# Optimization experiments

Hardware: AMD Instinct MI355X
Metric: run time of the kernel (lower is better)

The kernel has to match this reference:

```python
import jax, jax.numpy as jnp
import numpy as np
import math

LN_EPS = 1e-5

def _ln(x, g, b):
    m = jnp.mean(x, -1, keepdims=True)
    v = jnp.mean((x - m) ** 2, -1, keepdims=True)
    return (x - m) / jnp.sqrt(v + LN_EPS) * g + b

def setup_inputs() -> dict:
    key = jax.random.key(0)
    ks = jax.random.split(key, 16)
    B, N, D, V = 2, 512, 128, 16
    w = lambda k, shape: jax.random.normal(k, shape, jnp.float32) * 0.02
    return {
        "scalar": jax.random.normal(ks[0], (B, N, D), jnp.float32),
        "vector": jax.random.normal(ks[1], (B, N, 3, V), jnp.float32),
        "coords": jax.random.normal(ks[2], (B, N, 3), jnp.float32),
        "w_q": w(ks[3], (D, D)), "b_q": jnp.zeros((D,), jnp.float32),
        "w_k": w(ks[4], (D, D)), "b_k": jnp.zeros((D,), jnp.float32),
        "w_v": w(ks[5], (D, D)), "b_v": jnp.zeros((D,), jnp.float32),
        "w_d1": w(ks[6], (1, D)), "b_d1": jnp.zeros((D,), jnp.float32),
        "w_d2": w(ks[7], (D, D)), "b_d2": jnp.zeros((D,), jnp.float32),
        "w_g": w(ks[8], (D, V)), "b_g": jnp.zeros((V,), jnp.float32),
        "w_o": w(ks[9], (D, D)), "b_o": jnp.zeros((D,), jnp.float32),
        "w_f1": w(ks[10], (D, 2 * D)), "b_f1": jnp.zeros((2 * D,), jnp.float32),
        "w_f2": w(ks[11], (2 * D, D)), "b_f2": jnp.zeros((D,), jnp.float32),
        "w_vo": w(ks[12], (V, V)), "b_vo": jnp.zeros((V,), jnp.float32),
        "g_s": jnp.ones((D,), jnp.float32), "be_s": jnp.zeros((D,), jnp.float32),
        "g_v": jnp.ones((V,), jnp.float32), "be_v": jnp.zeros((V,), jnp.float32),
    }

def reference(scalar, vector, coords, w_q, b_q, w_k, b_k, w_v, b_v,
              w_d1, b_d1, w_d2, b_d2, w_g, b_g, w_o, b_o,
              w_f1, b_f1, w_f2, b_f2, w_vo, b_vo, g_s, be_s, g_v, be_v):
    D = scalar.shape[-1]
    # pairwise geometry: [B,N,N,3], [B,N,N,1]
    rel = coords[:, :, None, :] - coords[:, None, :, :]
    dist = jnp.linalg.norm(rel, axis=-1, keepdims=True)
    direction = rel / jnp.maximum(dist, 1e-6)
    sn = _ln(scalar, g_s, be_s)
    q = sn @ w_q + b_q
    k = sn @ w_k + b_k
    v = sn @ w_v + b_v
    # distance-conditioned bias: [B,N,N,D]
    bias = jax.nn.gelu(dist @ w_d1 + b_d1, approximate=False) @ w_d2 + b_d2
    # q_i . (k_j + bias_ij) / sqrt(D)
    logits = (jnp.einsum('bid,bjd->bij', q, k)
              + jnp.einsum('bid,bijd->bij', q, bias)) / math.sqrt(D)
    attn = jax.nn.softmax(logits, axis=-1)
    # sum_j attn_ij * (v_j + bias_ij)
    upd = jnp.einsum('bij,bjd->bid', attn, v) + jnp.einsum('bij,bijd->bid', attn, bias)
    scalar = scalar + (upd @ w_o + b_o)
    h = _ln(scalar, g_s, be_s)
    scalar = scalar + (jax.nn.gelu(h @ w_f1 + b_f1, approximate=False) @ w_f2 + b_f2)
    gate = jax.nn.sigmoid(scalar @ w_g + b_g)  # [B,N,V]
    # sum_j attn_ij * (vector_j + dir_ij * gate_i) decomposed (same math, no BxNxNx3xV tensor)
    agg = (jnp.einsum('bij,bjcv->bicv', attn, vector)
           + jnp.einsum('bij,bijc->bic', attn, direction)[..., None] * gate[:, :, None, :])
    projected = _ln(agg, g_v, be_v) @ w_vo + b_vo
    return scalar, vector + projected
```

## Files before the change

### kernel.cpp

```cpp
#include <hip/hip_runtime.h>
#include <math.h>

#define D 128
#define F 256
#define V 16
#define NSEQ 512
#define NROW 1024
#define MQ 7

__device__ __forceinline__ float gelu_exact(float x) {
    return 0.5f * x * (1.0f + erff(x * 0.70710678118654752f));
}

__device__ __forceinline__ float waveSum(float v) {
#pragma unroll
    for (int o = 32; o; o >>= 1) v += __shfl_xor(v, o);
    return v;
}
__device__ __forceinline__ float waveMax(float v) {
#pragma unroll
    for (int o = 32; o; o >>= 1) v = fmaxf(v, __shfl_xor(v, o));
    return v;
}

__device__ __forceinline__ void build_A(const float* __restrict__ w_d1,
                                        const float* __restrict__ b_d1,
                                        float* A_s, int t) {
    if (t < D) {
        const float gam[MQ] = {0.f, 0.5f, 0.39894228f, 0.f, -0.06649038f, 0.f,
                               0.0099735570f};
        float w = w_d1[t], b = b_d1[t];
        float wp[MQ], bp[MQ];
        wp[0] = 1.f; bp[0] = 1.f;
#pragma unroll
        for (int i = 1; i < MQ; i++) { wp[i] = wp[i - 1] * w; bp[i] = bp[i - 1] * b; }
        float A[MQ];
#pragma unroll
        for (int m = 0; m < MQ; m++) A[m] = 0.f;
#pragma unroll
        for (int k = 1; k < MQ; k++) {
            float g = gam[k];
            if (g == 0.f) continue;
            float C = 1.f;
            for (int m = 0; m <= k; m++) {
                A[m] = fmaf(g * C, wp[m] * bp[k - m], A[m]);
                C = C * (float)(k - m) / (float)(m + 1);
            }
        }
#pragma unroll
        for (int m = 0; m < MQ; m++) A_s[t * MQ + m] = A[m];
    }
}

__global__ __launch_bounds__(1024, 8) void k1_qkv(
    const float* __restrict__ scalar,
    const float* __restrict__ w_q, const float* __restrict__ b_q,
    const float* __restrict__ w_k, const float* __restrict__ b_k,
    const float* __restrict__ w_v, const float* __restrict__ b_v,
    const float* __restrict__ w_d1, const float* __restrict__ b_d1,
    const float* __restrict__ w_d2,
    const float* __restrict__ g_s, const float* __restrict__ be_s,
    float* __restrict__ qg, float* __restrict__ kTg, float* __restrict__ vg,
    float* __restrict__ Gg)
{
    const int t = threadIdx.x, wvid = t >> 6, ln = t & 63;
    const int r0 = blockIdx.x * 4;
    const int l = t & 127, rr = (t >> 7) & 3;
    __shared__ __align__(16) float snT[D][4];
    __shared__ float k_s[4][D];
    __shared__ __align__(16) float P3[3][8][4][D];
    __shared__ float redA[16], redB[16];
    float* A_s1 = &P3[0][0][0][0];

    float x = scalar[(size_t)(r0 + rr) * D + l];
    { float s = waveSum(x); if (ln == 0) redA[wvid] = s; }
    __syncthreads();
    float mean = (redA[2 * rr] + redA[2 * rr + 1]) * (1.0f / 128.0f);
    float dv = x - mean;
    { float s = waveSum(dv * dv); if (ln == 0) redB[wvid] = s; }
    __syncthreads();
    float var = (redB[2 * rr] + redB[2 * rr + 1]) * (1.0f / 128.0f);
    if (t < 512) snT[l][rr] = dv * rsqrtf(var + 1e-5f) * g_s[l] + be_s[l];
    __syncthreads();

    {
        const int eo = t >> 7, e0 = eo * 16;
        float aq0 = 0.f, aq1 = 0.f, aq2 = 0.f, aq3 = 0.f;
        float ak0 = 0.f, ak1 = 0.f, ak2 = 0.f, ak3 = 0.f;
        float av0 = 0.f, av1 = 0.f, av2 = 0.f, av3 = 0.f;
#pragma unroll 4
        for (int e = e0; e < e0 + 16; e++) {
            float4 s4 = *(const float4*)&snT[e][0];
            float wq = w_q[e * D + l], wk = w_k[e * D + l], wv = w_v[e * D + l];
            aq0 = fmaf(s4.x, wq, aq0); aq1 = fmaf(s4.y, wq, aq1);
            aq2 = fmaf(s4.z, wq, aq2); aq3 = fmaf(s4.w, wq, aq3);
            ak0 = fmaf(s4.x, wk, ak0); ak1 = fmaf(s4.y, wk, ak1);
            ak2 = fmaf(s4.z, wk, ak2); ak3 = fmaf(s4.w, wk, ak3);
            av0 = fmaf(s4.x, wv, av0); av1 = fmaf(s4.y, wv, av1);
            av2 = fmaf(s4.z, wv, av2); av3 = fmaf(s4.w, wv, av3);
        }
        P3[0][eo][0][l] = aq0; P3[0][eo][1][l] = aq1;
        P3[0][eo][2][l] = aq2; P3[0][eo][3][l] = aq3;
        P3[1][eo][0][l] = ak0; P3[1][eo][1][l] = ak1;
        P3[1][eo][2][l] = ak2; P3[1][eo][3][l] = ak3;
        P3[2][eo][0][l] = av0; P3[2][eo][1][l] = av1;
        P3[2][eo][2][l] = av2; P3[2][eo][3][l] = av3;
    }
    __syncthreads();

#pragma unroll
    for (int pass = 0; pass < 2; pass++) {
        const int o = t + pass * 1024;
        if (o < 1536) {
            const int mat = o >> 9, row = (o >> 7) & 3, l2 = o & 127;
            float acc = 0.f;
#pragma unroll
            for (int eo = 0; eo < 8; eo++) acc += P3[mat][eo][row][l2];
            if (mat == 0)      qg[(size_t)(r0 + row) * D + l2] = acc + b_q[l2];
            else if (mat == 1) k_s[row][l2] = acc + b_k[l2];
            else               vg[(size_t)(r0 + row) * D + l2] = acc + b_v[l2];
        }
    }
    __syncthreads();

    if (t < 128) {
        float4 kv = make_float4(k_s[0][t], k_s[1][t], k_s[2][t], k_s[3][t]);
        *(float4*)&kTg[(size_t)t * NROW + r0] = kv;
    }

    if (blockIdx.x == 0) {
        build_A(w_d1, b_d1, A_s1, t);
        __syncthreads();
        if (t < D * MQ) {
            const int m = t >> 7, l2 = t & 127;
            float acc = 0.f;
#pragma unroll 4
            for (int e = 0; e < D; e++)
                acc = fmaf(w_d2[e * D + l2], A_s1[e * MQ + m], acc);
            Gg[l2 * MQ + m] = acc;
        }
    }
}

__global__ __launch_bounds__(1024, 4) void k23(
    const float* __restrict__ coords, const float* __restrict__ vecin,
    const float* __restrict__ scalar,
    const float* __restrict__ qg, const float* __restrict__ kTg,
    const float* __restrict__ vg, const float* __restrict__ Gg,
    const float* __restrict__ b_d2,
    const float* __restrict__ w_o, const float* __restrict__ b_o,
    const float* __restrict__ w_f1, const float* __restrict__ b_f1,
    const float* __restrict__ w_f2, const float* __restrict__ b_f2,
    const float* __restrict__ w_g, const float* __restrict__ b_g,
    const float* __restrict__ w_vo, const float* __restrict__ b_vo,
    const float* __restrict__ g_s, const float* __restrict__ be_s,
    const float* __restrict__ g_v, const float* __restrict__ be_v,
    float* __restrict__ out_s, float* __restrict__ out_v)
{
    const int t = threadIdx.x, wvid = t >> 6, ln = t & 63;
    const int r0 = blockIdx.x * 4, b = blockIdx.x >> 7;
    __shared__ __align__(16) float AT[NSEQ * 4];
    __shared__ __align__(16) float PB[16384];
    __shared__ __align__(16) float qT[D][4];
    __shared__ float Gl[D * MQ];
    __shared__ float P_s[4][MQ];
    __shared__ __align__(16) float updT[D][4], hT[D][4], s1T[D][4];
    __shared__ __align__(16) float t2T[F][4];
    __shared__ float S_s[4][MQ], adir_s[4][3], avec_s[4][48];
    __shared__ float redA[16], redB[16], redC[16], redD[16];
    __shared__ float wredM[16][10], wredN[16][10];
    __shared__ float gate_s[4][V], gp[16][4][V], lnv_s[4][48];
    __shared__ __align__(16) float avp[16][4][48];

    if (t < 512) qT[t & 127][t >> 7] = qg[(size_t)(r0 + (t >> 7)) * D + (t & 127)];
    if (t < D * MQ) Gl[t] = Gg[t];
    __syncthreads();

    {
        const int dd = t & 127, row = (t >> 7) & 3;
        float qv = qT[dd][row];
        float pa[MQ];
#pragma unroll
        for (int m = 0; m < MQ; m++) pa[m] = qv * Gl[dd * MQ + m];
        pa[0] = fmaf(qv, b_d2[dd], pa[0]);
#pragma unroll
        for (int m = 0; m < MQ; m++) {
            float s = waveSum(pa[m]);
            if (ln == 0) wredM[wvid][m] = s;
        }
    }
    __syncthreads();
    if (t < 4 * MQ) {
        const int hh = t / MQ, m = t % MQ;
        P_s[hh][m] = (wredM[hh * 2][m] + wredM[hh * 2 + 1][m]
                    + wredM[8 + hh * 2][m] + wredM[8 + hh * 2 + 1][m]) * 0.5f;
    }

    {
        const int jq = t & 127, j0 = jq * 4, eq = t >> 7, e0 = eq * 16;
        const float* ke = kTg + (size_t)e0 * NROW + (size_t)b * NSEQ + j0;
        float acc[4][4];
#pragma unroll
        for (int i = 0; i < 4; i++)
#pragma unroll
            for (int k2 = 0; k2 < 4; k2++) acc[i][k2] = 0.f;
#pragma unroll 4
        for (int e = 0; e < 16; e++) {
            float4 kv = *(const float4*)&ke[(size_t)e * NROW];
            float4 q4 = *(const float4*)&qT[e0 + e][0];
            const float qr[4] = {q4.x, q4.y, q4.z, q4.w};
#pragma unroll
            for (int rr2 = 0; rr2 < 4; rr2++) {
                acc[rr2][0] = fmaf(qr[rr2], kv.x, acc[rr2][0]);
                acc[rr2][1] = fmaf(qr[rr2], kv.y, acc[rr2][1]);
                acc[rr2][2] = fmaf(qr[rr2], kv.z, acc[rr2][2]);
                acc[rr2][3] = fmaf(qr[rr2], kv.w, acc[rr2][3]);
            }
        }
#pragma unroll
        for (int rr2 = 0; rr2 < 4; rr2++)
            *(float4*)&PB[(eq * 4 + rr2) * 512 + j0] =
                make_float4(acc[rr2][0], acc[rr2][1], acc[rr2][2], acc[rr2][3]);
    }
    __syncthreads();

    const int h2 = t >> 9, j = t & 511;
    const int rA = r0 + h2, rB = rA + 2;
    const float* cj = coords + ((size_t)b * NSEQ + j) * 3;
    const float cjx = cj[0], cjy = cj[1], cjz = cj[2];
    float rxA = coords[(size_t)rA * 3 + 0] - cjx;
    float ryA = coords[(size_t)rA * 3 + 1] - cjy;
    float rzA = coords[(size_t)rA * 3 + 2] - cjz;
    float rxB = coords[(size_t)rB * 3 + 0] - cjx;
    float ryB = coords[(size_t)rB * 3 + 1] - cjy;
    float rzB = coords[(size_t)rB * 3 + 2] - cjz;
    float djA = sqrtf(rxA * rxA + ryA * ryA + rzA * rzA);
    float djB = sqrtf(rxB * rxB + ryB * ryB + rzB * rzB);
    float qkA = 0.f, qkB = 0.f;
#pragma unroll
    for (int eq = 0; eq < 8; eq++) {
        qkA += PB[(eq * 4 + h2) * 512 + j];
        qkB += PB[(eq * 4 + h2 + 2) * 512 + j];
    }
    float biasA = P_s[h2][MQ - 1], biasB = P_s[h2 + 2][MQ - 1];
#pragma unroll
    for (int m = MQ - 2; m >= 0; m--) {
        biasA = fmaf(biasA, djA, P_s[h2][m]);
        biasB = fmaf(biasB, djB, P_s[h2 + 2][m]);
    }
    const float sc = 0.08838834764831844f;
    float lgA = (qkA + biasA) * sc;
    float lgB = (qkB + biasB) * sc;

    {
        float m0 = waveMax(lgA), m1 = waveMax(lgB);
        if (ln == 0) { redA[wvid] = m0; redC[wvid] = m1; }
    }
    __syncthreads();
    float mxA = redA[8 * h2], mxB = redC[8 * h2];
#pragma unroll
    for (int k = 1; k < 8; k++) {
        mxA = fmaxf(mxA, redA[8 * h2 + k]);
        mxB = fmaxf(mxB, redC[8 * h2 + k]);
    }
    float pA = __expf(lgA - mxA), pB = __expf(lgB - mxB);
    {
        float s0 = waveSum(pA), s1 = waveSum(pB);
        if (ln == 0) { redB[wvid] = s0; redD[wvid] = s1; }
    }
    __syncthreads();
    float lsA = 0.f, lsB = 0.f;
#pragma unroll
    for (int k = 0; k < 8; k++) { lsA += redB[8 * h2 + k]; lsB += redD[8 * h2 + k]; }
    float aA = pA / lsA, aB = pB / lsB;
    AT[j * 4 + h2] = aA;
    AT[j * 4 + h2 + 2] = aB;

    {
        float red[10], red2[10];
        float w0 = aA, w1 = aB;
#pragma unroll
        for (int m = 0; m < MQ; m++) { red[m] = w0; w0 *= djA; red2[m] = w1; w1 *= djB; }
        float iaA = aA * __builtin_amdgcn_rcpf(fmaxf(djA, 1e-6f));
        float iaB = aB * __builtin_amdgcn_rcpf(fmaxf(djB, 1e-6f));
        red[7] = iaA * rxA; red[8] = iaA * ryA; red[9] = iaA * rzA;
        red2[7] = iaB * rxB; red2[8] = iaB * ryB; red2[9] = iaB * rzB;
#pragma unroll
        for (int m = 0; m < 10; m++) {
            float s = waveSum(red[m]);
            float s2 = waveSum(red2[m]);
            if (ln == 0) { wredM[wvid][m] = s; wredN[wvid][m] = s2; }
        }
    }
    __syncthreads();
    if (t < 40) {
        const int hh = t / 10, m = t % 10;
        float s = 0.f;
        if (hh < 2) {
#pragma unroll
            for (int k = 0; k < 8; k++) s += wredM[8 * hh + k][m];
        } else {
#pragma unroll
            for (int k = 0; k < 8; k++) s += wredN[8 * (hh - 2) + k][m];
        }
        if (m < MQ) S_s[hh][m] = s;
        else        adir_s[hh][m - MQ] = s;
    }

    {
        const int dq = t & 31, d0 = dq * 4, jo = t >> 5, jb = 16 * jo;
        const float* vb = vg + ((size_t)b * NSEQ + jb) * D + d0;
        float acc[4][4];
#pragma unroll
        for (int i = 0; i < 4; i++)
#pragma unroll
            for (int k2 = 0; k2 < 4; k2++) acc[i][k2] = 0.f;
#pragma unroll 4
        for (int jj = 0; jj < 16; jj++) {
            float4 at = *(const float4*)&AT[(jb + jj) * 4];
            float4 vv = *(const float4*)&vb[(size_t)jj * D];
            const float ar[4] = {at.x, at.y, at.z, at.w};
#pragma unroll
            for (int rr2 = 0; rr2 < 4; rr2++) {
                acc[rr2][0] = fmaf(ar[rr2], vv.x, acc[rr2][0]);
                acc[rr2][1] = fmaf(ar[rr2], vv.y, acc[rr2][1]);
                acc[rr2][2] = fmaf(ar[rr2], vv.z, acc[rr2][2]);
                acc[rr2][3] = fmaf(ar[rr2], vv.w, acc[rr2][3]);
            }
        }
#pragma unroll
        for (int rr2 = 0; rr2 < 4; rr2++)
            *(float4*)&PB[(jo * 4 + rr2) * 128 + d0] =
                make_float4(acc[rr2][0], acc[rr2][1], acc[rr2][2], acc[rr2][3]);
    }
    if (ln < 48) {
        const int jb = 32 * wvid;
        const float* vp = vecin + ((size_t)b * NSEQ + jb) * 48 + ln;
        float c[4] = {0.f, 0.f, 0.f, 0.f};
#pragma unroll 4
        for (int jj = 0; jj < 32; jj++) {
            float4 at = *(const float4*)&AT[(jb + jj) * 4];
            float vv = vp[(size_t)jj * 48];
            c[0] = fmaf(at.x, vv, c[0]);
            c[1] = fmaf(at.y, vv, c[1]);
            c[2] = fmaf(at.z, vv, c[2]);
            c[3] = fmaf(at.w, vv, c[3]);
        }
#pragma unroll
        for (int rr2 = 0; rr2 < 4; rr2++) avp[wvid][rr2][ln] = c[rr2];
    }
    __syncthreads();

    if (t < 512) {
        const int row = t >> 7, l = t & 127;
        float acc = 0.f;
#pragma unroll
        for (int jo = 0; jo < 32; jo++) acc += PB[(jo * 4 + row) * 128 + l];
        float aa = 0.f;
#pragma unroll
        for (int m = 0; m < MQ; m++) aa = fmaf(Gl[l * MQ + m], S_s[row][m], aa);
        updT[l][row] = acc + aa + b_d2[l];
    } else if (t - 512 < 192) {
        const int idx = t - 512, row = idx / 48, i2 = idx % 48;
        float s = 0.f;
#pragma unroll
        for (int w2 = 0; w2 < 16; w2++) s += avp[w2][row][i2];
        avec_s[row][i2] = s;
    }
    __syncthreads();

    {
        const int eo = t >> 7, l = t & 127, e0 = 16 * eo;
        float c[4] = {0.f, 0.f, 0.f, 0.f};
#pragma unroll 4
        for (int e = e0; e < e0 + 16; e++) {
            float4 up = *(const float4*)&updT[e][0];
            float wv = w_o[e * D + l];
            c[0] = fmaf(up.x, wv, c[0]); c[1] = fmaf(up.y, wv, c[1]);
            c[2] = fmaf(up.z, wv, c[2]); c[3] = fmaf(up.w, wv, c[3]);
        }
#pragma unroll
        for (int rr2 = 0; rr2 < 4; rr2++) PB[(eo * 4 + rr2) * 128 + l] = c[rr2];
    }
    __syncthreads();
    float xln = 0.f;
    {
        const int row = (t >> 7) & 3, l = t & 127;
        if (t < 512) {
            float acc = 0.f;
#pragma unroll
            for (int eo = 0; eo < 8; eo++) acc += PB[(eo * 4 + row) * 128 + l];
            xln = scalar[(size_t)(r0 + row) * D + l] + acc + b_o[l];
            s1T[l][row] = xln;
        }
        float s = waveSum(xln);
        if (t < 512 && ln == 0) redA[wvid] = s;
    }
    __syncthreads();
    float dvv = 0.f;
    if (t < 512) {
        const int row = (t >> 7) & 3;
        float mean = (redA[2 * row] + redA[2 * row + 1]) * (1.0f / 128.0f);
        dvv = xln - mean;
    }
    {
        float s = waveSum(dvv * dvv);
        if (t < 512 && ln == 0) redB[wvid] = s;
    }
    __syncthreads();
    if (t < 512) {
        const int row = (t >> 7) & 3, l = t & 127;
        float var = (redB[2 * row] + redB[2 * row + 1]) * (1.0f / 128.0f);
        hT[l][row] = dvv * rsqrtf(var + 1e-5f) * g_s[l] + be_s[l];
    }
    __syncthreads();

    {
        const int f = t & 255, eq = t >> 8, e0 = 32 * eq;
        float c[4] = {0.f, 0.f, 0.f, 0.f};
#pragma unroll 4
        for (int e = e0; e < e0 + 32; e++) {
            float4 hv = *(const float4*)&hT[e][0];
            float wv = w_f1[e * F + f];
            c[0] = fmaf(hv.x, wv, c[0]); c[1] = fmaf(hv.y, wv, c[1]);
            c[2] = fmaf(hv.z, wv, c[2]); c[3] = fmaf(hv.w, wv, c[3]);
        }
#pragma unroll
        for (int rr2 = 0; rr2 < 4; rr2++) PB[(eq * 4 + rr2) * 256 + f] = c[rr2];
    }
    __syncthreads();
    {
        const int row = t >> 8, f = t & 255;
        float acc = 0.f;
#pragma unroll
        for (int eq = 0; eq < 4; eq++) acc += PB[(eq * 4 + row) * 256 + f];
        t2T[f][row] = gelu_exact(acc + b_f1[f]);
    }
    __syncthreads();

    {
        const int fo = t >> 7, l = t & 127, f0 = 32 * fo;
        float c[4] = {0.f, 0.f, 0.f, 0.f};
#pragma unroll 4
        for (int f = f0; f < f0 + 32; f++) {
            float4 tv = *(const float4*)&t2T[f][0];
            float wv = w_f2[f * D + l];
            c[0] = fmaf(tv.x, wv, c[0]); c[1] = fmaf(tv.y, wv, c[1]);
            c[2] = fmaf(tv.z, wv, c[2]); c[3] = fmaf(tv.w, wv, c[3]);
        }
#pragma unroll
        for (int rr2 = 0; rr2 < 4; rr2++) PB[(fo * 4 + rr2) * 128 + l] = c[rr2];
    }
    __syncthreads();
    if (t < 512) {
        const int row = t >> 7, l = t & 127;
        float acc = 0.f;
#pragma unroll
        for (int fo = 0; fo < 8; fo++) acc += PB[(fo * 4 + row) * 128 + l];
        float v2 = s1T[l][row] + acc + b_f2[l];
        out_s[(size_t)(r0 + row) * D + l] = v2;
        s1T[l][row] = v2;
    }
    __syncthreads();

    {
        const int vv = t & 15, row = (t >> 4) & 3, dg = t >> 6, d0 = 8 * dg;
        float aa = 0.f;
#pragma unroll
        for (int dd = d0; dd < d0 + 8; dd++)
            aa = fmaf(s1T[dd][row], w_g[dd * V + vv], aa);
        gp[dg][row][vv] = aa;
    }
    __syncthreads();
    if (t < 64) {
        const int row = t >> 4, vv = t & 15;
        float aa = b_g[vv];
#pragma unroll
        for (int dg = 0; dg < 16; dg++) aa += gp[dg][row][vv];
        gate_s[row][vv] = 1.0f / (1.0f + __expf(-aa));
    }
    __syncthreads();

    if (t < 192) {
        const int row = t / 48, idx = t % 48, c = idx >> 4, vv = idx & 15;
        float agg = avec_s[row][idx] + adir_s[row][c] * gate_s[row][vv];
        float s = agg;
#pragma unroll
        for (int o = 8; o; o >>= 1) s += __shfl_xor(s, o, 16);
        float mean = s * (1.0f / 16.0f);
        float e = agg - mean;
        float s2 = e * e;
#pragma unroll
        for (int o = 8; o; o >>= 1) s2 += __shfl_xor(s2, o, 16);
        float rstd = rsqrtf(s2 * (1.0f / 16.0f) + 1e-5f);
        lnv_s[row][idx] = e * rstd * g_v[vv] + be_v[vv];
    }
    __syncthreads();
    if (t < 192) {
        const int row = t / 48, idx = t % 48, c = idx >> 4, vv = idx & 15;
        const int rw = r0 + row;
        float aa = b_vo[vv];
#pragma unroll
        for (int w2 = 0; w2 < V; w2++)
            aa = fmaf(lnv_s[row][c * V + w2], w_vo[w2 * V + vv], aa);
        out_v[(size_t)rw * 48 + idx] = vecin[(size_t)rw * 48 + idx] + aa;
    }
}

extern "C" void kernel_launch(void* const* d_in, const int* in_sizes, int n_in,
                              void* d_out, int out_size, void* d_ws, size_t ws_size,
                              hipStream_t stream)
{
    (void)in_sizes; (void)n_in; (void)out_size; (void)ws_size;
    const float* scalar = (const float*)d_in[0];
    const float* vecin  = (const float*)d_in[1];
    const float* coords = (const float*)d_in[2];
    const float* w_q  = (const float*)d_in[3];  const float* b_q  = (const float*)d_in[4];
    const float* w_k  = (const float*)d_in[5];  const float* b_k  = (const float*)d_in[6];
    const float* w_v  = (const float*)d_in[7];  const float* b_v  = (const float*)d_in[8];
    const float* w_d1 = (const float*)d_in[9];  const float* b_d1 = (const float*)d_in[10];
    const float* w_d2 = (const float*)d_in[11]; const float* b_d2 = (const float*)d_in[12];
    const float* w_g  = (const float*)d_in[13]; const float* b_g  = (const float*)d_in[14];
    const float* w_o  = (const float*)d_in[15]; const float* b_o  = (const float*)d_in[16];
    const float* w_f1 = (const float*)d_in[17]; const float* b_f1 = (const float*)d_in[18];
    const float* w_f2 = (const float*)d_in[19]; const float* b_f2 = (const float*)d_in[20];
    const float* w_vo = (const float*)d_in[21]; const float* b_vo = (const float*)d_in[22];
    const float* g_s  = (const float*)d_in[23]; const float* be_s = (const float*)d_in[24];
    const float* g_v  = (const float*)d_in[25]; const float* be_v = (const float*)d_in[26];

    float* ws  = (float*)d_ws;
    float* qg  = ws;
    float* kTg = ws + 131072;
    float* vg  = ws + 262144;
    float* Gg  = ws + 393216;

    float* out_s = (float*)d_out;
    float* out_v = out_s + 131072;

    hipLaunchKernelGGL(k1_qkv, dim3(NROW / 4), dim3(1024), 0, stream,
                       scalar, w_q, b_q, w_k, b_k, w_v, b_v, w_d1, b_d1,
                       w_d2, g_s, be_s, qg, kTg, vg, Gg);
    hipLaunchKernelGGL(k23, dim3(NROW / 4), dim3(1024), 0, stream,
                       coords, vecin, scalar, qg, kTg, vg, Gg,
                       b_d2, w_o, b_o, w_f1, b_f1, w_f2, b_f2,
                       w_g, b_g, w_vo, b_vo, g_s, be_s, g_v, be_v,
                       out_s, out_v);
}
```

Measured before the change: 150.6 us.

## Retile QKV projection, split G build across blocks, prefetch vector rows, simplify softmax mapping

The QKV projection in k1 is retiled so each thread computes a 4x4 register tile with float4 weight loads over one matrix, using 768 threads instead of all 1024 doing three matrices. The G matrix build is spread over MQ blocks, one column each, instead of being serialised in block 0. In k23 each thread now handles one row with two j positions, so the softmax and moment reductions run in a single pass instead of duplicated A/B reductions. The per-wave vector rows are also prefetched into registers at kernel start. The extra 32-float register array and the changed reduction mapping may raise register pressure in a 1024-thread block.

```diff
diff --git a/kernel.cpp b/kernel.cpp
--- a/kernel.cpp
+++ b/kernel.cpp
@@ -69,8 +69,8 @@
     __shared__ __align__(16) float snT[D][4];
     __shared__ float k_s[4][D];
     __shared__ __align__(16) float P3[3][8][4][D];
+    __shared__ float A_sG[D * MQ];
     __shared__ float redA[16], redB[16];
-    float* A_s1 = &P3[0][0][0][0];
 
     float x = scalar[(size_t)(r0 + rr) * D + l];
     { float s = waveSum(x); if (ln == 0) redA[wvid] = s; }
@@ -83,28 +83,35 @@
     if (t < 512) snT[l][rr] = dv * rsqrtf(var + 1e-5f) * g_s[l] + be_s[l];
     __syncthreads();
 
-    {
-        const int eo = t >> 7, e0 = eo * 16;
-        float aq0 = 0.f, aq1 = 0.f, aq2 = 0.f, aq3 = 0.f;
-        float ak0 = 0.f, ak1 = 0.f, ak2 = 0.f, ak3 = 0.f;
-        float av0 = 0.f, av1 = 0.f, av2 = 0.f, av3 = 0.f;
+    if (t < 768) {
+        const int g = t >> 7;
+        const int mat = (g < 3) ? g : g - 3, eh = (g < 3) ? 0 : 1;
+        const int es = (t >> 5) & 3, lq = t & 31, l0 = lq * 4;
+        const int e0 = eh * 64 + es * 16;
+        const float* W = (mat == 0) ? w_q : (mat == 1) ? w_k : w_v;
+        float acc[4][4];
+#pragma unroll
+        for (int r2 = 0; r2 < 4; r2++)
+#pragma unroll
+            for (int c2 = 0; c2 < 4; c2++) acc[r2][c2] = 0.f;
 #pragma unroll 4
         for (int e = e0; e < e0 + 16; e++) {
+            float4 w4 = *(const float4*)&W[e * D + l0];
             float4 s4 = *(const float4*)&snT[e][0];
-            float wq = w_q[e * D + l], wk = w_k[e * D + l], wv = w_v[e * D + l];
-            aq0 = fmaf(s4.x, wq, aq0); aq1 = fmaf(s4.y, wq, aq1);
-            aq2 = fmaf(s4.z, wq, aq2); aq3 = fmaf(s4.w, wq, aq3);
-            ak0 = fmaf(s4.x, wk, ak0); ak1 = fmaf(s4.y, wk, ak1);
-            ak2 = fmaf(s4.z, wk, ak2); ak3 = fmaf(s4.w, wk, ak3);
-            av0 = fmaf(s4.x, wv, av0); av1 = fmaf(s4.y, wv, av1);
-            av2 = fmaf(s4.z, wv, av2); av3 = fmaf(s4.w, wv, av3);
-        }
-        P3[0][eo][0][l] = aq0; P3[0][eo][1][l] = aq1;
-        P3[0][eo][2][l] = aq2; P3[0][eo][3][l] = aq3;
-        P3[1][eo][0][l] = ak0; P3[1][eo][1][l] = ak1;
-        P3[1][eo][2][l] = ak2; P3[1][eo][3][l] = ak3;
-        P3[2][eo][0][l] = av0; P3[2][eo][1][l] = av1;
-        P3[2][eo][2][l] = av2; P3[2][eo][3][l] = av3;
+            const float sr[4] = {s4.x, s4.y, s4.z, s4.w};
+#pragma unroll
+            for (int r2 = 0; r2 < 4; r2++) {
+                acc[r2][0] = fmaf(sr[r2], w4.x, acc[r2][0]);
+                acc[r2][1] = fmaf(sr[r2], w4.y, acc[r2][1]);
+                acc[r2][2] = fmaf(sr[r2], w4.z, acc[r2][2]);
+                acc[r2][3] = fmaf(sr[r2], w4.w, acc[r2][3]);
+            }
+        }
+        const int pi = eh * 4 + es;
+#pragma unroll
+        for (int r2 = 0; r2 < 4; r2++)
+            *(float4*)&P3[mat][pi][r2][l0] =
+                make_float4(acc[r2][0], acc[r2][1], acc[r2][2], acc[r2][3]);
     }
     __syncthreads();
 
@@ -128,16 +135,16 @@
         *(float4*)&kTg[(size_t)t * NROW + r0] = kv;
     }
 
-    if (blockIdx.x == 0) {
-        build_A(w_d1, b_d1, A_s1, t);
+    if (blockIdx.x < MQ) {
+        build_A(w_d1, b_d1, A_sG, t);
         __syncthreads();
-        if (t < D * MQ) {
-            const int m = t >> 7, l2 = t & 127;
+        const int m = blockIdx.x;
+        if (t < D) {
             float acc = 0.f;
 #pragma unroll 4
             for (int e = 0; e < D; e++)
-                acc = fmaf(w_d2[e * D + l2], A_s1[e * MQ + m], acc);
-            Gg[l2 * MQ + m] = acc;
+                acc = fmaf(w_d2[e * D + t], A_sG[e * MQ + m], acc);
+            Gg[t * MQ + m] = acc;
         }
     }
 }
@@ -167,10 +174,17 @@
     __shared__ __align__(16) float updT[D][4], hT[D][4], s1T[D][4];
     __shared__ __align__(16) float t2T[F][4];
     __shared__ float S_s[4][MQ], adir_s[4][3], avec_s[4][48];
-    __shared__ float redA[16], redB[16], redC[16], redD[16];
-    __shared__ float wredM[16][10], wredN[16][10];
+    __shared__ float redA[16], redB[16];
+    __shared__ float wredM[16][10];
     __shared__ float gate_s[4][V], gp[16][4][V], lnv_s[4][48];
     __shared__ __align__(16) float avp[16][4][48];
+
+    float vpre[32];
+    if (ln < 48) {
+        const float* vp = vecin + ((size_t)b * NSEQ + 32 * wvid) * 48 + ln;
+#pragma unroll
+        for (int jj = 0; jj < 32; jj++) vpre[jj] = vp[(size_t)jj * 48];
+    }
 
     if (t < 512) qT[t & 127][t >> 7] = qg[(size_t)(r0 + (t >> 7)) * D + (t & 127)];
     if (t < D * MQ) Gl[t] = Gg[t];
@@ -224,85 +238,68 @@
     }
     __syncthreads();
 
-    const int h2 = t >> 9, j = t & 511;
-    const int rA = r0 + h2, rB = rA + 2;
-    const float* cj = coords + ((size_t)b * NSEQ + j) * 3;
-    const float cjx = cj[0], cjy = cj[1], cjz = cj[2];
-    float rxA = coords[(size_t)rA * 3 + 0] - cjx;
-    float ryA = coords[(size_t)rA * 3 + 1] - cjy;
-    float rzA = coords[(size_t)rA * 3 + 2] - cjz;
-    float rxB = coords[(size_t)rB * 3 + 0] - cjx;
-    float ryB = coords[(size_t)rB * 3 + 1] - cjy;
-    float rzB = coords[(size_t)rB * 3 + 2] - cjz;
-    float djA = sqrtf(rxA * rxA + ryA * ryA + rzA * rzA);
-    float djB = sqrtf(rxB * rxB + ryB * ryB + rzB * rzB);
-    float qkA = 0.f, qkB = 0.f;
+    const int row = t >> 8, jh = t & 255;
+    const int rA = r0 + row;
+    const float cix = coords[(size_t)rA * 3 + 0];
+    const float ciy = coords[(size_t)rA * 3 + 1];
+    const float ciz = coords[(size_t)rA * 3 + 2];
+    const float* cj0 = coords + ((size_t)b * NSEQ + jh) * 3;
+    const float* cj1 = cj0 + 256 * 3;
+    float rx0 = cix - cj0[0], ry0 = ciy - cj0[1], rz0 = ciz - cj0[2];
+    float rx1 = cix - cj1[0], ry1 = ciy - cj1[1], rz1 = ciz - cj1[2];
+    float dj0 = sqrtf(rx0 * rx0 + ry0 * ry0 + rz0 * rz0);
+    float dj1 = sqrtf(rx1 * rx1 + ry1 * ry1 + rz1 * rz1);
+    float qk0 = 0.f, qk1 = 0.f;
 #pragma unroll
     for (int eq = 0; eq < 8; eq++) {
-        qkA += PB[(eq * 4 + h2) * 512 + j];
-        qkB += PB[(eq * 4 + h2 + 2) * 512 + j];
-    }
-    float biasA = P_s[h2][MQ - 1], biasB = P_s[h2 + 2][MQ - 1];
+        qk0 += PB[(eq * 4 + row) * 512 + jh];
+        qk1 += PB[(eq * 4 + row) * 512 + jh + 256];
+    }
+    float bias0 = P_s[row][MQ - 1], bias1 = bias0;
 #pragma unroll
     for (int m = MQ - 2; m >= 0; m--) {
-        biasA = fmaf(biasA, djA, P_s[h2][m]);
-        biasB = fmaf(biasB, djB, P_s[h2 + 2][m]);
+        bias0 = fmaf(bias0, dj0, P_s[row][m]);
+        bias1 = fmaf(bias1, dj1, P_s[row][m]);
     }
     const float sc = 0.08838834764831844f;
-    float lgA = (qkA + biasA) * sc;
-    float lgB = (qkB + biasB) * sc;
-
-    {
-        float m0 = waveMax(lgA), m1 = waveMax(lgB);
-        if (ln == 0) { redA[wvid] = m0; redC[wvid] = m1; }
-    }
-    __syncthreads();
-    float mxA = redA[8 * h2], mxB = redC[8 * h2];
-#pragma unroll
-    for (int k = 1; k < 8; k++) {
-        mxA = fmaxf(mxA, redA[8 * h2 + k]);
-        mxB = fmaxf(mxB, redC[8 * h2 + k]);
-    }
-    float pA = __expf(lgA - mxA), pB = __expf(lgB - mxB);
-    {
-        float s0 = waveSum(pA), s1 = waveSum(pB);
-        if (ln == 0) { redB[wvid] = s0; redD[wvid] = s1; }
-    }
-    __syncthreads();
-    float lsA = 0.f, lsB = 0.f;
-#pragma unroll
-    for (int k = 0; k < 8; k++) { lsA += redB[8 * h2 + k]; lsB += redD[8 * h2 + k]; }
-    float aA = pA / lsA, aB = pB / lsB;
-    AT[j * 4 + h2] = aA;
-    AT[j * 4 + h2 + 2] = aB;
-
-    {
-        float red[10], red2[10];
-        float w0 = aA, w1 = aB;
-#pragma unroll
-        for (int m = 0; m < MQ; m++) { red[m] = w0; w0 *= djA; red2[m] = w1; w1 *= djB; }
-        float iaA = aA * __builtin_amdgcn_rcpf(fmaxf(djA, 1e-6f));
-        float iaB = aB * __builtin_amdgcn_rcpf(fmaxf(djB, 1e-6f));
-        red[7] = iaA * rxA; red[8] = iaA * ryA; red[9] = iaA * rzA;
-        red2[7] = iaB * rxB; red2[8] = iaB * ryB; red2[9] = iaB * rzB;
+    float lg0 = (qk0 + bias0) * sc;
+    float lg1 = (qk1 + bias1) * sc;
+
+    { float mx = waveMax(fmaxf(lg0, lg1)); if (ln == 0) redA[wvid] = mx; }
+    __syncthreads();
+    float mx = fmaxf(fmaxf(redA[4 * row], redA[4 * row + 1]),
+                     fmaxf(redA[4 * row + 2], redA[4 * row + 3]));
+    float p0 = __expf(lg0 - mx), p1 = __expf(lg1 - mx);
+    { float s = waveSum(p0 + p1); if (ln == 0) redB[wvid] = s; }
+    __syncthreads();
+    float ls = redB[4 * row] + redB[4 * row + 1]
+             + redB[4 * row + 2] + redB[4 * row + 3];
+    float inv = 1.0f / ls;
+    float a0 = p0 * inv, a1 = p1 * inv;
+    AT[jh * 4 + row] = a0;
+    AT[(jh + 256) * 4 + row] = a1;
+
+    {
+        float red[10];
+        float w0 = a0, w1 = a1;
+#pragma unroll
+        for (int m = 0; m < MQ; m++) { red[m] = w0 + w1; w0 *= dj0; w1 *= dj1; }
+        float ia0 = a0 * __builtin_amdgcn_rcpf(fmaxf(dj0, 1e-6f));
+        float ia1 = a1 * __builtin_amdgcn_rcpf(fmaxf(dj1, 1e-6f));
+        red[7] = ia0 * rx0 + ia1 * rx1;
+        red[8] = ia0 * ry0 + ia1 * ry1;
+        red[9] = ia0 * rz0 + ia1 * rz1;
 #pragma unroll
         for (int m = 0; m < 10; m++) {
             float s = waveSum(red[m]);
-            float s2 = waveSum(red2[m]);
-            if (ln == 0) { wredM[wvid][m] = s; wredN[wvid][m] = s2; }
+            if (ln == 0) wredM[wvid][m] = s;
         }
     }
     __syncthreads();
     if (t < 40) {
         const int hh = t / 10, m = t % 10;
-        float s = 0.f;
-        if (hh < 2) {
-#pragma unroll
-            for (int k = 0; k < 8; k++) s += wredM[8 * hh + k][m];
-        } else {
-#pragma unroll
-            for (int k = 0; k < 8; k++) s += wredN[8 * (hh - 2) + k][m];
-        }
+        float s = wredM[4 * hh][m] + wredM[4 * hh + 1][m]
+                + wredM[4 * hh + 2][m] + wredM[4 * hh + 3][m];
         if (m < MQ) S_s[hh][m] = s;
         else        adir_s[hh][m - MQ] = s;
     }
@@ -335,16 +332,14 @@
     }
     if (ln < 48) {
         const int jb = 32 * wvid;
-        const float* vp = vecin + ((size_t)b * NSEQ + jb) * 48 + ln;
         float c[4] = {0.f, 0.f, 0.f, 0.f};
-#pragma unroll 4
+#pragma unroll
         for (int jj = 0; jj < 32; jj++) {
             float4 at = *(const float4*)&AT[(jb + jj) * 4];
-            float vv = vp[(size_t)jj * 48];
-            c[0] = fmaf(at.x, vv, c[0]);
-            c[1] = fmaf(at.y, vv, c[1]);
-            c[2] = fmaf(at.z, vv, c[2]);
-            c[3] = fmaf(at.w, vv, c[3]);
+            c[0] = fmaf(at.x, vpre[jj], c[0]);
+            c[1] = fmaf(at.y, vpre[jj], c[1]);
+            c[2] = fmaf(at.z, vpre[jj], c[2]);
+            c[3] = fmaf(at.w, vpre[jj], c[3]);
         }
 #pragma unroll
         for (int rr2 = 0; rr2 < 4; rr2++) avp[wvid][rr2][ln] = c[rr2];
@@ -352,20 +347,20 @@
     __syncthreads();
 
     if (t < 512) {
-        const int row = t >> 7, l = t & 127;
+        const int rw = t >> 7, l = t & 127;
         float acc = 0.f;
 #pragma unroll
-        for (int jo = 0; jo < 32; jo++) acc += PB[(jo * 4 + row) * 128 + l];
+        for (int jo = 0; jo < 32; jo++) acc += PB[(jo * 4 + rw) * 128 + l];
         float aa = 0.f;
 #pragma unroll
-        for (int m = 0; m < MQ; m++) aa = fmaf(Gl[l * MQ + m], S_s[row][m], aa);
-        updT[l][row] = acc + aa + b_d2[l];
+        for (int m = 0; m < MQ; m++) aa = fmaf(Gl[l * MQ + m], S_s[rw][m], aa);
+        updT[l][rw] = acc + aa + b_d2[l];
     } else if (t - 512 < 192) {
-        const int idx = t - 512, row = idx / 48, i2 = idx % 48;
+        const int idx = t - 512, rw = idx / 48, i2 = idx % 48;
         float s = 0.f;
 #pragma unroll
-        for (int w2 = 0; w2 < 16; w2++) s += avp[w2][row][i2];
-        avec_s[row][i2] = s;
+        for (int w2 = 0; w2 < 16; w2++) s += avp[w2][rw][i2];
+        avec_s[rw][i2] = s;
     }
     __syncthreads();
 
@@ -385,13 +380,13 @@
     __syncthreads();
     float xln = 0.f;
     {
-        const int row = (t >> 7) & 3, l = t & 127;
+        const int rw = (t >> 7) & 3, l = t & 127;
         if (t < 512) {
             float acc = 0.f;
 #pragma unroll
-            for (int eo = 0; eo < 8; eo++) acc += PB[(eo * 4 + row) * 128 + l];
-            xln = scalar[(size_t)(r0 + row) * D + l] + acc + b_o[l];
-            s1T[l][row] = xln;
+            for (int eo = 0; eo < 8; eo++) acc += PB[(eo * 4 + rw) * 128 + l];
+            xln = scalar[(size_t)(r0 + rw) * D + l] + acc + b_o[l];
+            s1T[l][rw] = xln;
         }
         float s = waveSum(xln);
         if (t < 512 && ln == 0) redA[wvid] = s;
@@ -399,8 +394,8 @@
     __syncthreads();
     float dvv = 0.f;
     if (t < 512) {
-        const int row = (t >> 7) & 3;
-        float mean = (redA[2 * row] + redA[2 * row + 1]) * (1.0f / 128.0f);
+        const int rw = (t >> 7) & 3;
+        float mean = (redA[2 * rw] + redA[2 * rw + 1]) * (1.0f / 128.0f);
         dvv = xln - mean;
     }
     {
@@ -409,9 +404,9 @@
     }
     __syncthreads();
     if (t < 512) {
-        const int row = (t >> 7) & 3, l = t & 127;
-        float var = (redB[2 * row] + redB[2 * row + 1]) * (1.0f / 128.0f);
-        hT[l][row] = dvv * rsqrtf(var + 1e-5f) * g_s[l] + be_s[l];
+        const int rw = (t >> 7) & 3, l = t & 127;
+        float var = (redB[2 * rw] + redB[2 * rw + 1]) * (1.0f / 128.0f);
+        hT[l][rw] = dvv * rsqrtf(var + 1e-5f) * g_s[l] + be_s[l];
     }
     __syncthreads();
 
@@ -430,11 +425,11 @@
     }
     __syncthreads();
     {
-        const int row = t >> 8, f = t & 255;
+        const int rw = t >> 8, f = t & 255;
         float acc = 0.f;
 #pragma unroll
-        for (int eq = 0; eq < 4; eq++) acc += PB[(eq * 4 + row) * 256 + f];
-        t2T[f][row] = gelu_exact(acc + b_f1[f]);
+        for (int eq = 0; eq < 4; eq++) acc += PB[(eq * 4 + rw) * 256 + f];
+        t2T[f][rw] = gelu_exact(acc + b_f1[f]);
     }
     __syncthreads();
 
@@ -453,37 +448,37 @@
     }
     __syncthreads();
     if (t < 512) {
-        const int row = t >> 7, l = t & 127;
+        const int rw = t >> 7, l = t & 127;
         float acc = 0.f;
 #pragma unroll
-        for (int fo = 0; fo < 8; fo++) acc += PB[(fo * 4 + row) * 128 + l];
-        float v2 = s1T[l][row] + acc + b_f2[l];
-        out_s[(size_t)(r0 + row) * D + l] = v2;
-        s1T[l][row] = v2;
-    }
-    __syncthreads();
-
-    {
-        const int vv = t & 15, row = (t >> 4) & 3, dg = t >> 6, d0 = 8 * dg;
+        for (int fo = 0; fo < 8; fo++) acc += PB[(fo * 4 + rw) * 128 + l];
+        float v2 = s1T[l][rw] + acc + b_f2[l];
+        out_s[(size_t)(r0 + rw) * D + l] = v2;
+        s1T[l][rw] = v2;
+    }
+    __syncthreads();
+
+    {
+        const int vv = t & 15, rw = (t >> 4) & 3, dg = t >> 6, d0 = 8 * dg;
         float aa = 0.f;
 #pragma unroll
         for (int dd = d0; dd < d0 + 8; dd++)
-            aa = fmaf(s1T[dd][row], w_g[dd * V + vv], aa);
-        gp[dg][row][vv] = aa;
+            aa = fmaf(s1T[dd][rw], w_g[dd * V + vv], aa);
+        gp[dg][rw][vv] = aa;
     }
     __syncthreads();
     if (t < 64) {
-        const int row = t >> 4, vv = t & 15;
+        const int rw = t >> 4, vv = t & 15;
         float aa = b_g[vv];
 #pragma unroll
-        for (int dg = 0; dg < 16; dg++) aa += gp[dg][row][vv];
-        gate_s[row][vv] = 1.0f / (1.0f + __expf(-aa));
+        for (int dg = 0; dg < 16; dg++) aa += gp[dg][rw][vv];
+        gate_s[rw][vv] = 1.0f / (1.0f + __expf(-aa));
     }
     __syncthreads();
 
     if (t < 192) {
-        const int row = t / 48, idx = t % 48, c = idx >> 4, vv = idx & 15;
-        float agg = avec_s[row][idx] + adir_s[row][c] * gate_s[row][vv];
+        const int rw = t / 48, idx = t % 48, c = idx >> 4, vv = idx & 15;
+        float agg = avec_s[rw][idx] + adir_s[rw][c] * gate_s[rw][vv];
         float s = agg;
 #pragma unroll
         for (int o = 8; o; o >>= 1) s += __shfl_xor(s, o, 16);
@@ -493,17 +488,17 @@
 #pragma unroll
         for (int o = 8; o; o >>= 1) s2 += __shfl_xor(s2, o, 16);
         float rstd = rsqrtf(s2 * (1.0f / 16.0f) + 1e-5f);
-        lnv_s[row][idx] = e * rstd * g_v[vv] + be_v[vv];
+        lnv_s[rw][idx] = e * rstd * g_v[vv] + be_v[vv];
     }
     __syncthreads();
     if (t < 192) {
-        const int row = t / 48, idx = t % 48, c = idx >> 4, vv = idx & 15;
-        const int rw = r0 + row;
+        const int rw = t / 48, idx = t % 48, c = idx >> 4, vv = idx & 15;
+        const int rwg = r0 + rw;
         float aa = b_vo[vv];
 #pragma unroll
         for (int w2 = 0; w2 < V; w2++)
-            aa = fmaf(lnv_s[row][c * V + w2], w_vo[w2 * V + vv], aa);
-        out_v[(size_t)rw * 48 + idx] = vecin[(size_t)rw * 48 + idx] + aa;
+            aa = fmaf(lnv_s[rw][c * V + w2], w_vo[w2 * V + vv], aa);
+        out_v[(size_t)rwg * 48 + idx] = vecin[(size_t)rwg * 48 + idx] + aa;
     }
 }
 
```

New measurement: 149.8 us, median of 2. No clear change (-0.6%).
